# Performance work log

Measured on AMD Instinct MI355X. Metric: run time of the kernel, lower is better.

The kernel has to match this reference:

```python
import jax, jax.numpy as jnp
import numpy as np

LN_EPS = 1e-5


def setup_inputs() -> dict:
    key = jax.random.key(0)
    ks = jax.random.split(key, 4)
    B, L, Dm, N = 16, 2048, 512, 64
    return {
        "x": jax.random.normal(ks[0], (B, L, Dm), dtype=jnp.float32),
        "A": jax.random.normal(ks[1], (Dm, N), dtype=jnp.float32),
        "C": jax.random.normal(ks[2], (Dm, N), dtype=jnp.float32),
        "D": jax.random.normal(ks[3], (Dm,), dtype=jnp.float32),
        "gamma": jnp.ones((Dm,), dtype=jnp.float32),
        "beta": jnp.zeros((Dm,), dtype=jnp.float32),
    }


def reference(x, A, C, D, gamma, beta):
    # LayerNorm over last dim (matches nn.LayerNorm(d_model))
    mean = jnp.mean(x, axis=-1, keepdims=True)
    var = jnp.mean(jnp.square(x - mean), axis=-1, keepdims=True)
    x_norm = (x - mean) * jax.lax.rsqrt(var + LN_EPS) * gamma + beta

    B, L, Dm = x.shape
    N = A.shape[1]
    h0 = jnp.zeros((B, N), dtype=x.dtype)

    def step(h, u):
        # u: [B, Dm]; h: [B, N]
        h = jnp.tanh(u @ A + h)
        y = h @ C.T + u * D  # [B, Dm]
        return h, y

    # scan over time: xs [L, B, Dm]
    _, ys = jax.lax.scan(step, h0, jnp.swapaxes(x_norm, 0, 1))
    out = jnp.swapaxes(ys, 0, 1)  # [B, L, Dm]
    return out + x
```

## Files before the change

kernel.cpp:

```cpp
#include <hip/hip_runtime.h>
#include <hip/hip_bf16.h>

typedef short bf16x8 __attribute__((ext_vector_type(8)));
typedef float f32x4 __attribute__((ext_vector_type(4)));

constexpr int B_ = 16;
constexpr int L_ = 2048;
constexpr int DM = 512;
constexpr int NS = 64;
constexpr int BL = B_ * L_;
constexpr float LN_EPS = 1e-5f;
constexpr float KLN = 2.8853900817779268f;

constexpr int SEGS = 32;
constexpr int LSEG = L_ / SEGS;
constexpr int WARM = 64;

__device__ __forceinline__ unsigned f32bits(float f) {
    union { float f; unsigned u; } v{f}; return v.u;
}
__device__ __forceinline__ float bitsf32(unsigned u) {
    union { unsigned u; float f; } v{u}; return v.f;
}
__device__ __forceinline__ unsigned short f2bf(float f) {
    unsigned u = f32bits(f);
    unsigned r = u + 0x7FFF + ((u >> 16) & 1);
    return (unsigned short)(r >> 16);
}

__device__ __forceinline__ void norm_split8(float4 u0, float4 u1,
                                            float rstd, float m2,
                                            bf16x8& ah, bf16x8& al) {
    float t[8] = { fmaf(u0.x, rstd, m2), fmaf(u0.y, rstd, m2),
                   fmaf(u0.z, rstd, m2), fmaf(u0.w, rstd, m2),
                   fmaf(u1.x, rstd, m2), fmaf(u1.y, rstd, m2),
                   fmaf(u1.z, rstd, m2), fmaf(u1.w, rstd, m2) };
    unsigned hb[8], lb[8];
    #pragma unroll
    for (int j = 0; j < 8; ++j) {
        unsigned tb = f32bits(t[j]);
        hb[j] = tb & 0xFFFF0000u;
        lb[j] = f32bits(t[j] - bitsf32(hb[j]));
    }
    union { unsigned u[4]; bf16x8 v; } H, L;
    #pragma unroll
    for (int p = 0; p < 4; ++p) {
        H.u[p] = (hb[2*p] >> 16) | hb[2*p+1];
        L.u[p] = (lb[2*p] >> 16) | (lb[2*p+1] & 0xFFFF0000u);
    }
    ah = H.v; al = L.v;
}

__global__ __launch_bounds__(256) void k_pack(const float* __restrict__ A,
                                              const float* __restrict__ C,
                                              const float* __restrict__ gamma,
                                              const float* __restrict__ beta,
                                              const float* __restrict__ Dv,
                                              unsigned short* __restrict__ PAh,
                                              unsigned short* __restrict__ PAl,
                                              unsigned short* __restrict__ PC2,
                                              float* __restrict__ c0,
                                              float* __restrict__ gd,
                                              float* __restrict__ bd) {
    const int blk = blockIdx.x;
    const int tid = threadIdx.x;
    if (blk < 32) {
        const int g = blk * 256 + tid;
        if (g < 4096) {
            const int lane = g & 63, ct = (g >> 6) & 3, k32 = (g >> 8) & 3, kc = g >> 10;
            const int kbase = kc * 128 + k32 * 32 + (lane >> 4) * 8;
            const int col   = ct * 16 + (lane & 15);
            unsigned hb[8], lb[8];
            #pragma unroll
            for (int j = 0; j < 8; ++j) {
                float v = gamma[kbase + j] * A[(size_t)(kbase + j) * NS + col];
                unsigned tb = f32bits(v);
                hb[j] = tb & 0xFFFF0000u;
                lb[j] = f32bits(v - bitsf32(hb[j]));
            }
            uint4 ph, pl;
            ph.x = (hb[0] >> 16) | hb[1]; ph.y = (hb[2] >> 16) | hb[3];
            ph.z = (hb[4] >> 16) | hb[5]; ph.w = (hb[6] >> 16) | hb[7];
            pl.x = (lb[0] >> 16) | (lb[1] & 0xFFFF0000u);
            pl.y = (lb[2] >> 16) | (lb[3] & 0xFFFF0000u);
            pl.z = (lb[4] >> 16) | (lb[5] & 0xFFFF0000u);
            pl.w = (lb[6] >> 16) | (lb[7] & 0xFFFF0000u);
            *reinterpret_cast<uint4*>(PAh + (size_t)g * 8) = ph;
            *reinterpret_cast<uint4*>(PAl + (size_t)g * 8) = pl;
        } else {
            const int g2   = g - 4096;
            const int lane = g2 & 63;
            const int kt   = (g2 >> 6) & 1;
            const int offs = (g2 >> 7) & 1;
            const int dblk = g2 >> 8;
            const int i    = lane & 15;
            const int d    = dblk * 32 + ((i >> 2) * 8) + offs * 4 + (i & 3);
            const int nb   = kt * 32 + (lane >> 4) * 8;
            unsigned short v[8];
            #pragma unroll
            for (int j = 0; j < 8; ++j) v[j] = f2bf(C[(size_t)d * NS + nb + j]);
            uint4 p;
            p.x = v[0] | ((unsigned)v[1] << 16); p.y = v[2] | ((unsigned)v[3] << 16);
            p.z = v[4] | ((unsigned)v[5] << 16); p.w = v[6] | ((unsigned)v[7] << 16);
            *reinterpret_cast<uint4*>(PC2 + (size_t)g2 * 8) = p;
        }
    } else {
        __shared__ float red[256];
        #pragma unroll
        for (int i = 0; i < 2; ++i) {
            int d = tid + 256 * i;
            gd[d] = gamma[d] * Dv[d];
            bd[d] = beta[d] * Dv[d];
        }
        const int n = tid & 63, part = tid >> 6;
        float s = 0.f;
        #pragma unroll 8
        for (int k = part * 128; k < part * 128 + 128; ++k)
            s += beta[k] * A[(size_t)k * NS + n];
        red[tid] = s;
        __syncthreads();
        if (tid < 64)
            c0[tid] = red[tid] + red[tid + 64] + red[tid + 128] + red[tid + 192];
    }
}

__global__ __launch_bounds__(256) void k_gemmA(const float* __restrict__ x,
                                               const unsigned short* __restrict__ PAh,
                                               const unsigned short* __restrict__ PAl,
                                               const float* __restrict__ c0,
                                               float* __restrict__ stats,
                                               float* __restrict__ Bu) {
    const int tid  = threadIdx.x;
    const int r0   = blockIdx.x * 64;
    const int w    = tid >> 6;
    const int lane = tid & 63;
    const int myrow = 16 * w + (lane & 15);
    const int kb    = (lane >> 4) * 8;
    const float* xrow = x + (size_t)(r0 + myrow) * DM;

    float s = 0.f, s2 = 0.f;
    #pragma unroll
    for (int kc = 0; kc < 4; ++kc) {
        #pragma unroll
        for (int k32 = 0; k32 < 4; ++k32) {
            float4 a = *reinterpret_cast<const float4*>(xrow + kc * 128 + k32 * 32 + kb);
            float4 b = *reinterpret_cast<const float4*>(xrow + kc * 128 + k32 * 32 + kb + 4);
            s  += (a.x + a.y) + (a.z + a.w) + (b.x + b.y) + (b.z + b.w);
            s2 += a.x*a.x + a.y*a.y + a.z*a.z + a.w*a.w
                + b.x*b.x + b.y*b.y + b.z*b.z + b.w*b.w;
        }
    }
    s += __shfl_xor(s, 16); s2 += __shfl_xor(s2, 16);
    s += __shfl_xor(s, 32); s2 += __shfl_xor(s2, 32);
    const float mean = s * (1.0f / DM);
    const float var  = s2 * (1.0f / DM) - mean * mean;
    const float rstd = rsqrtf(var + LN_EPS);
    const float m2   = -mean * rstd;
    if (lane < 16) {
        stats[2 * (r0 + myrow)]     = mean;
        stats[2 * (r0 + myrow) + 1] = rstd;
    }

    f32x4 acc[4] = {};
    const bf16x8* ABh = reinterpret_cast<const bf16x8*>(PAh);
    const bf16x8* ABl = reinterpret_cast<const bf16x8*>(PAl);
    #pragma unroll
    for (int kc = 0; kc < 4; ++kc) {
        #pragma unroll
        for (int k32 = 0; k32 < 4; ++k32) {
            float4 u0 = *reinterpret_cast<const float4*>(xrow + kc * 128 + k32 * 32 + kb);
            float4 u1 = *reinterpret_cast<const float4*>(xrow + kc * 128 + k32 * 32 + kb + 4);
            bf16x8 ah, al;
            norm_split8(u0, u1, rstd, m2, ah, al);
            #pragma unroll
            for (int ct = 0; ct < 4; ++ct) {
                const int fi = ((kc * 4 + k32) * 4 + ct) * 64 + lane;
                bf16x8 bh = ABh[fi];
                bf16x8 bl = ABl[fi];
                acc[ct] = __builtin_amdgcn_mfma_f32_16x16x32_bf16(ah, bh, acc[ct], 0, 0, 0);
                acc[ct] = __builtin_amdgcn_mfma_f32_16x16x32_bf16(ah, bl, acc[ct], 0, 0, 0);
                acc[ct] = __builtin_amdgcn_mfma_f32_16x16x32_bf16(al, bh, acc[ct], 0, 0, 0);
            }
        }
    }

    const int orow = r0 + 16 * w + (lane >> 4) * 4;
    #pragma unroll
    for (int ct = 0; ct < 4; ++ct) {
        const int n = ct * 16 + (lane & 15);
        const float c0n = c0[n];
        #pragma unroll
        for (int j = 0; j < 4; ++j)
            Bu[(size_t)(orow + j) * NS + n] = acc[ct][j] + c0n;
    }
}

__global__ __launch_bounds__(512, 4) void k_scanC(const float* __restrict__ x,
                                                  const unsigned short* __restrict__ PC2,
                                                  const float* __restrict__ gd,
                                                  const float* __restrict__ bd,
                                                  const float* __restrict__ stats,
                                                  const float* __restrict__ Bu,
                                                  float* __restrict__ out) {
    __shared__ __align__(16) char smem[8192 + 4096];
    const int tid = threadIdx.x;
    const int seg = blockIdx.x & (SEGS - 1);
    const int b   = blockIdx.x >> 5;
    const int l0  = seg * LSEG;
    const int rowbase = b * L_ + l0;

    if (tid < 64) {
        constexpr int G = 16;
        const int n     = tid;
        const int start = (seg == 0) ? 0 : (l0 - WARM);
        const int skip  = l0 - start;
        const int nGrp  = (l0 + LSEG - start) / G;
        const float* bp = Bu + ((size_t)b * L_ + start) * NS + n;
        char* hbase = smem;

        float bufA[G], bufB[G];
        #pragma unroll
        for (int j = 0; j < G; ++j) bufA[j] = KLN * bp[(size_t)j * NS];
        float hv = 0.0f;
        int g = 0;
        for (;;) {
            {
                if (g + 1 < nGrp) {
                    const int base = (g + 1) * G;
                    #pragma unroll
                    for (int j = 0; j < G; ++j)
                        bufB[j] = KLN * bp[(size_t)(base + j) * NS];
                }
                const int lbase = g * G - skip;
                const bool doStore = lbase >= 0;
                #pragma unroll
                for (int j = 0; j < G; ++j) {
                    float t = fmaf(hv, KLN, bufA[j]);
                    float e = __builtin_amdgcn_exp2f(t);
                    float rr = __builtin_amdgcn_rcpf(e + 1.0f);
                    hv = fmaf(-2.0f, rr, 1.0f);
                    if (doStore) {
                        const int lr = lbase + j;
                        *reinterpret_cast<unsigned short*>(
                            hbase + lr * 128 + ((2 * n) ^ ((lr & 7) << 4))) = f2bf(hv);
                    }
                }
            }
            if (++g == nGrp) break;
            {
                if (g + 1 < nGrp) {
                    const int base = (g + 1) * G;
                    #pragma unroll
                    for (int j = 0; j < G; ++j)
                        bufA[j] = KLN * bp[(size_t)(base + j) * NS];
                }
                const int lbase = g * G - skip;
                const bool doStore = lbase >= 0;
                #pragma unroll
                for (int j = 0; j < G; ++j) {
                    float t = fmaf(hv, KLN, bufB[j]);
                    float e = __builtin_amdgcn_exp2f(t);
                    float rr = __builtin_amdgcn_rcpf(e + 1.0f);
                    hv = fmaf(-2.0f, rr, 1.0f);
                    if (doStore) {
                        const int lr = lbase + j;
                        *reinterpret_cast<unsigned short*>(
                            hbase + lr * 128 + ((2 * n) ^ ((lr & 7) << 4))) = f2bf(hv);
                    }
                }
            }
            if (++g == nGrp) break;
        }
    } else {
        float* GdS = (float*)(smem + 8192);
        const int t2 = tid - 64;
        if (t2 < 256)
            reinterpret_cast<float4*>(GdS)[t2] =
                (t2 < 128) ? reinterpret_cast<const float4*>(gd)[t2]
                           : reinterpret_cast<const float4*>(bd)[t2 - 128];
    }
    __syncthreads();

    const int w    = tid >> 6;
    const int lane = tid & 63;
    const int rg   = w & 3;
    const int half = w >> 2;
    const int hr   = rg * 16 + (lane & 15);
    const int kb   = (lane >> 4) * 8;
    const int grow = rowbase + hr;
    const float mean = stats[2 * grow];
    const float rstd = stats[2 * grow + 1];

    bf16x8 hfr0 = *reinterpret_cast<const bf16x8*>(
        smem + hr * 128 + (((lane >> 4) * 16) ^ ((hr & 7) << 4)));
    bf16x8 hfr1 = *reinterpret_cast<const bf16x8*>(
        smem + hr * 128 + ((64 + (lane >> 4) * 16) ^ ((hr & 7) << 4)));

    const float* GdS = (const float*)(smem + 8192);
    const float* BdS = GdS + DM;
    const float* xrp = x + (size_t)grow * DM;
    float* orp = out + (size_t)grow * DM;

    #pragma unroll
    for (int i = 0; i < 8; ++i) {
        const int dblk = half * 8 + i;
        bf16x8 c00 = *reinterpret_cast<const bf16x8*>(PC2 + ((size_t)dblk * 256 + lane) * 8);
        bf16x8 c01 = *reinterpret_cast<const bf16x8*>(PC2 + ((size_t)dblk * 256 + 64 + lane) * 8);
        bf16x8 c10 = *reinterpret_cast<const bf16x8*>(PC2 + ((size_t)dblk * 256 + 128 + lane) * 8);
        bf16x8 c11 = *reinterpret_cast<const bf16x8*>(PC2 + ((size_t)dblk * 256 + 192 + lane) * 8);
        f32x4 a0 = {}, a1 = {};
        a0 = __builtin_amdgcn_mfma_f32_16x16x32_bf16(c00, hfr0, a0, 0, 0, 0);
        a0 = __builtin_amdgcn_mfma_f32_16x16x32_bf16(c01, hfr1, a0, 0, 0, 0);
        a1 = __builtin_amdgcn_mfma_f32_16x16x32_bf16(c10, hfr0, a1, 0, 0, 0);
        a1 = __builtin_amdgcn_mfma_f32_16x16x32_bf16(c11, hfr1, a1, 0, 0, 0);

        const int db = dblk * 32 + kb;
        const float4 x0 = *reinterpret_cast<const float4*>(xrp + db);
        const float4 x1 = *reinterpret_cast<const float4*>(xrp + db + 4);
        const float4 g0 = *reinterpret_cast<const float4*>(GdS + db);
        const float4 g1 = *reinterpret_cast<const float4*>(GdS + db + 4);
        const float4 d0 = *reinterpret_cast<const float4*>(BdS + db);
        const float4 d1 = *reinterpret_cast<const float4*>(BdS + db + 4);
        float4 o0, o1;
        o0.x = fmaf((x0.x - mean) * rstd, g0.x, a0[0] + d0.x + x0.x);
        o0.y = fmaf((x0.y - mean) * rstd, g0.y, a0[1] + d0.y + x0.y);
        o0.z = fmaf((x0.z - mean) * rstd, g0.z, a0[2] + d0.z + x0.z);
        o0.w = fmaf((x0.w - mean) * rstd, g0.w, a0[3] + d0.w + x0.w);
        o1.x = fmaf((x1.x - mean) * rstd, g1.x, a1[0] + d1.x + x1.x);
        o1.y = fmaf((x1.y - mean) * rstd, g1.y, a1[1] + d1.y + x1.y);
        o1.z = fmaf((x1.z - mean) * rstd, g1.z, a1[2] + d1.z + x1.z);
        o1.w = fmaf((x1.w - mean) * rstd, g1.w, a1[3] + d1.w + x1.w);
        *reinterpret_cast<float4*>(orp + db)     = o0;
        *reinterpret_cast<float4*>(orp + db + 4) = o1;
    }
}

extern "C" void kernel_launch(void* const* d_in, const int* in_sizes, int n_in,
                              void* d_out, int out_size, void* d_ws, size_t ws_size,
                              hipStream_t stream) {
    const float* x     = (const float*)d_in[0];
    const float* A     = (const float*)d_in[1];
    const float* C     = (const float*)d_in[2];
    const float* Dv    = (const float*)d_in[3];
    const float* gamma = (const float*)d_in[4];
    const float* beta  = (const float*)d_in[5];
    float* out = (float*)d_out;

    char* ws = (char*)d_ws;
    float* Bu           = (float*)(ws);
    float* stats        = (float*)(ws + (size_t)BL * NS * 4);
    char* p = ws + (size_t)BL * NS * 4 + (size_t)BL * 2 * 4;
    unsigned short* PAh = (unsigned short*)p;        p += (size_t)DM * NS * 2;
    unsigned short* PAl = (unsigned short*)p;        p += (size_t)DM * NS * 2;
    unsigned short* PC2 = (unsigned short*)p;        p += (size_t)DM * NS * 2;
    float* c0           = (float*)p;                 p += 256;
    float* gd           = (float*)p;                 p += (size_t)DM * 4;
    float* bd           = (float*)p;

    k_pack<<<33, 256, 0, stream>>>(A, C, gamma, beta, Dv, PAh, PAl, PC2, c0, gd, bd);
    k_gemmA<<<BL / 64, 256, 0, stream>>>(x, PAh, PAl, c0, stats, Bu);
    k_scanC<<<B_ * SEGS, 512, 0, stream>>>(x, PC2, gd, bd, stats, Bu, out);
}
```

Before: 68.93 us.

## Fuse LayerNorm/A-projection GEMM into scan kernel, keeping Bu and stats in LDS

Merges the A-projection GEMM kernel into the segmented scan kernel. Each block computes LayerNorm statistics and the projection for its segment plus warm-up rows directly into shared memory, then runs the recurrence and the C-projection epilogue. This removes the global round trip of Bu and stats and one kernel launch. In exchange the warm-up rows' GEMM is recomputed per segment (128 rows instead of 64), LDS use grows to about 47KB per block which may lower occupancy, and the GEMM phase now serialises with the scan inside each block.

```diff
diff --git a/kernel.cpp b/kernel.cpp
--- a/kernel.cpp
+++ b/kernel.cpp
@@ -124,114 +124,111 @@
     }
 }
 
-__global__ __launch_bounds__(256) void k_gemmA(const float* __restrict__ x,
-                                               const unsigned short* __restrict__ PAh,
-                                               const unsigned short* __restrict__ PAl,
-                                               const float* __restrict__ c0,
-                                               float* __restrict__ stats,
-                                               float* __restrict__ Bu) {
+__global__ __launch_bounds__(512, 4) void k_all(const float* __restrict__ x,
+                                                const unsigned short* __restrict__ PAh,
+                                                const unsigned short* __restrict__ PAl,
+                                                const unsigned short* __restrict__ PC2,
+                                                const float* __restrict__ c0,
+                                                const float* __restrict__ gd,
+                                                const float* __restrict__ bd,
+                                                float* __restrict__ out) {
+    __shared__ __align__(16) char smem[33792 + 8192 + 4096 + 1024];
+    float* BuS          = (float*)smem;
+    char*  hbase        = smem + 33792;
+    float* GdS          = (float*)(smem + 33792 + 8192);
+    float* BdS          = GdS + DM;
+    float* statsS       = (float*)(smem + 33792 + 8192 + 4096);
+
     const int tid  = threadIdx.x;
-    const int r0   = blockIdx.x * 64;
+    const int blk  = blockIdx.x;
+    const int seg  = blk & (SEGS - 1);
+    const int b    = blk >> 5;
+    const int l0   = seg * LSEG;
+    const int lstart   = (seg == 0) ? 0 : (l0 - WARM);
+    const int nrows    = l0 + LSEG - lstart;
+    const int liveBase = nrows - 64;
+
     const int w    = tid >> 6;
     const int lane = tid & 63;
     const int myrow = 16 * w + (lane & 15);
     const int kb    = (lane >> 4) * 8;
-    const float* xrow = x + (size_t)(r0 + myrow) * DM;
-
-    float s = 0.f, s2 = 0.f;
-    #pragma unroll
-    for (int kc = 0; kc < 4; ++kc) {
-        #pragma unroll
-        for (int k32 = 0; k32 < 4; ++k32) {
-            float4 a = *reinterpret_cast<const float4*>(xrow + kc * 128 + k32 * 32 + kb);
-            float4 b = *reinterpret_cast<const float4*>(xrow + kc * 128 + k32 * 32 + kb + 4);
-            s  += (a.x + a.y) + (a.z + a.w) + (b.x + b.y) + (b.z + b.w);
-            s2 += a.x*a.x + a.y*a.y + a.z*a.z + a.w*a.w
-                + b.x*b.x + b.y*b.y + b.z*b.z + b.w*b.w;
-        }
-    }
-    s += __shfl_xor(s, 16); s2 += __shfl_xor(s2, 16);
-    s += __shfl_xor(s, 32); s2 += __shfl_xor(s2, 32);
-    const float mean = s * (1.0f / DM);
-    const float var  = s2 * (1.0f / DM) - mean * mean;
-    const float rstd = rsqrtf(var + LN_EPS);
-    const float m2   = -mean * rstd;
-    if (lane < 16) {
-        stats[2 * (r0 + myrow)]     = mean;
-        stats[2 * (r0 + myrow) + 1] = rstd;
-    }
-
-    f32x4 acc[4] = {};
-    const bf16x8* ABh = reinterpret_cast<const bf16x8*>(PAh);
-    const bf16x8* ABl = reinterpret_cast<const bf16x8*>(PAl);
-    #pragma unroll
-    for (int kc = 0; kc < 4; ++kc) {
-        #pragma unroll
-        for (int k32 = 0; k32 < 4; ++k32) {
-            float4 u0 = *reinterpret_cast<const float4*>(xrow + kc * 128 + k32 * 32 + kb);
-            float4 u1 = *reinterpret_cast<const float4*>(xrow + kc * 128 + k32 * 32 + kb + 4);
-            bf16x8 ah, al;
-            norm_split8(u0, u1, rstd, m2, ah, al);
-            #pragma unroll
-            for (int ct = 0; ct < 4; ++ct) {
-                const int fi = ((kc * 4 + k32) * 4 + ct) * 64 + lane;
-                bf16x8 bh = ABh[fi];
-                bf16x8 bl = ABl[fi];
-                acc[ct] = __builtin_amdgcn_mfma_f32_16x16x32_bf16(ah, bh, acc[ct], 0, 0, 0);
-                acc[ct] = __builtin_amdgcn_mfma_f32_16x16x32_bf16(ah, bl, acc[ct], 0, 0, 0);
-                acc[ct] = __builtin_amdgcn_mfma_f32_16x16x32_bf16(al, bh, acc[ct], 0, 0, 0);
-            }
-        }
-    }
-
-    const int orow = r0 + 16 * w + (lane >> 4) * 4;
-    #pragma unroll
-    for (int ct = 0; ct < 4; ++ct) {
-        const int n = ct * 16 + (lane & 15);
-        const float c0n = c0[n];
-        #pragma unroll
-        for (int j = 0; j < 4; ++j)
-            Bu[(size_t)(orow + j) * NS + n] = acc[ct][j] + c0n;
-    }
-}
-
-__global__ __launch_bounds__(512, 4) void k_scanC(const float* __restrict__ x,
-                                                  const unsigned short* __restrict__ PC2,
-                                                  const float* __restrict__ gd,
-                                                  const float* __restrict__ bd,
-                                                  const float* __restrict__ stats,
-                                                  const float* __restrict__ Bu,
-                                                  float* __restrict__ out) {
-    __shared__ __align__(16) char smem[8192 + 4096];
-    const int tid = threadIdx.x;
-    const int seg = blockIdx.x & (SEGS - 1);
-    const int b   = blockIdx.x >> 5;
-    const int l0  = seg * LSEG;
-    const int rowbase = b * L_ + l0;
-
-    if (tid < 64) {
+
+    if (w * 16 < nrows) {
+        const float* xrow = x + ((size_t)b * L_ + lstart + myrow) * DM;
+
+        float s = 0.f, s2 = 0.f;
+        #pragma unroll
+        for (int kc = 0; kc < 4; ++kc) {
+            #pragma unroll
+            for (int k32 = 0; k32 < 4; ++k32) {
+                float4 a = *reinterpret_cast<const float4*>(xrow + kc * 128 + k32 * 32 + kb);
+                float4 bq = *reinterpret_cast<const float4*>(xrow + kc * 128 + k32 * 32 + kb + 4);
+                s  += (a.x + a.y) + (a.z + a.w) + (bq.x + bq.y) + (bq.z + bq.w);
+                s2 += a.x*a.x + a.y*a.y + a.z*a.z + a.w*a.w
+                    + bq.x*bq.x + bq.y*bq.y + bq.z*bq.z + bq.w*bq.w;
+            }
+        }
+        s += __shfl_xor(s, 16); s2 += __shfl_xor(s2, 16);
+        s += __shfl_xor(s, 32); s2 += __shfl_xor(s2, 32);
+        const float mean = s * (1.0f / DM);
+        const float var  = s2 * (1.0f / DM) - mean * mean;
+        const float rstd = rsqrtf(var + LN_EPS);
+        const float m2   = -mean * rstd;
+        if (lane < 16) {
+            statsS[2 * myrow]     = mean;
+            statsS[2 * myrow + 1] = rstd;
+        }
+
+        f32x4 acc[4] = {};
+        const bf16x8* ABh = reinterpret_cast<const bf16x8*>(PAh);
+        const bf16x8* ABl = reinterpret_cast<const bf16x8*>(PAl);
+        #pragma unroll
+        for (int kc = 0; kc < 4; ++kc) {
+            #pragma unroll
+            for (int k32 = 0; k32 < 4; ++k32) {
+                float4 u0 = *reinterpret_cast<const float4*>(xrow + kc * 128 + k32 * 32 + kb);
+                float4 u1 = *reinterpret_cast<const float4*>(xrow + kc * 128 + k32 * 32 + kb + 4);
+                bf16x8 ah, al;
+                norm_split8(u0, u1, rstd, m2, ah, al);
+                #pragma unroll
+                for (int ct = 0; ct < 4; ++ct) {
+                    const int fi = ((kc * 4 + k32) * 4 + ct) * 64 + lane;
+                    bf16x8 bh = ABh[fi];
+                    bf16x8 bl = ABl[fi];
+                    acc[ct] = __builtin_amdgcn_mfma_f32_16x16x32_bf16(ah, bh, acc[ct], 0, 0, 0);
+                    acc[ct] = __builtin_amdgcn_mfma_f32_16x16x32_bf16(ah, bl, acc[ct], 0, 0, 0);
+                    acc[ct] = __builtin_amdgcn_mfma_f32_16x16x32_bf16(al, bh, acc[ct], 0, 0, 0);
+                }
+            }
+        }
+        const int orow = 16 * w + (lane >> 4) * 4;
+        #pragma unroll
+        for (int ct = 0; ct < 4; ++ct) {
+            const int n = ct * 16 + (lane & 15);
+            const float c0n = c0[n];
+            #pragma unroll
+            for (int j = 0; j < 4; ++j)
+                BuS[(orow + j) * 66 + n] = acc[ct][j] + c0n;
+        }
+    }
+    __syncthreads();
+
+    if (w == 0) {
         constexpr int G = 16;
-        const int n     = tid;
-        const int start = (seg == 0) ? 0 : (l0 - WARM);
-        const int skip  = l0 - start;
-        const int nGrp  = (l0 + LSEG - start) / G;
-        const float* bp = Bu + ((size_t)b * L_ + start) * NS + n;
-        char* hbase = smem;
-
+        const int nGrp = nrows / G;
         float bufA[G], bufB[G];
         #pragma unroll
-        for (int j = 0; j < G; ++j) bufA[j] = KLN * bp[(size_t)j * NS];
+        for (int j = 0; j < G; ++j) bufA[j] = KLN * BuS[j * 66 + lane];
         float hv = 0.0f;
         int g = 0;
         for (;;) {
             {
                 if (g + 1 < nGrp) {
-                    const int base = (g + 1) * G;
                     #pragma unroll
                     for (int j = 0; j < G; ++j)
-                        bufB[j] = KLN * bp[(size_t)(base + j) * NS];
-                }
-                const int lbase = g * G - skip;
+                        bufB[j] = KLN * BuS[((g + 1) * G + j) * 66 + lane];
+                }
+                const int lbase = g * G - liveBase;
                 const bool doStore = lbase >= 0;
                 #pragma unroll
                 for (int j = 0; j < G; ++j) {
@@ -242,19 +239,18 @@
                     if (doStore) {
                         const int lr = lbase + j;
                         *reinterpret_cast<unsigned short*>(
-                            hbase + lr * 128 + ((2 * n) ^ ((lr & 7) << 4))) = f2bf(hv);
+                            hbase + lr * 128 + ((2 * lane) ^ ((lr & 7) << 4))) = f2bf(hv);
                     }
                 }
             }
             if (++g == nGrp) break;
             {
                 if (g + 1 < nGrp) {
-                    const int base = (g + 1) * G;
                     #pragma unroll
                     for (int j = 0; j < G; ++j)
-                        bufA[j] = KLN * bp[(size_t)(base + j) * NS];
-                }
-                const int lbase = g * G - skip;
+                        bufA[j] = KLN * BuS[((g + 1) * G + j) * 66 + lane];
+                }
+                const int lbase = g * G - liveBase;
                 const bool doStore = lbase >= 0;
                 #pragma unroll
                 for (int j = 0; j < G; ++j) {
@@ -265,14 +261,13 @@
                     if (doStore) {
                         const int lr = lbase + j;
                         *reinterpret_cast<unsigned short*>(
-                            hbase + lr * 128 + ((2 * n) ^ ((lr & 7) << 4))) = f2bf(hv);
+                            hbase + lr * 128 + ((2 * lane) ^ ((lr & 7) << 4))) = f2bf(hv);
                     }
                 }
             }
             if (++g == nGrp) break;
         }
     } else {
-        float* GdS = (float*)(smem + 8192);
         const int t2 = tid - 64;
         if (t2 < 256)
             reinterpret_cast<float4*>(GdS)[t2] =
@@ -281,25 +276,20 @@
     }
     __syncthreads();
 
-    const int w    = tid >> 6;
-    const int lane = tid & 63;
     const int rg   = w & 3;
     const int half = w >> 2;
     const int hr   = rg * 16 + (lane & 15);
-    const int kb   = (lane >> 4) * 8;
-    const int grow = rowbase + hr;
-    const float mean = stats[2 * grow];
-    const float rstd = stats[2 * grow + 1];
+    const size_t grow = (size_t)b * L_ + l0 + hr;
+    const float mean = statsS[2 * (liveBase + hr)];
+    const float rstd = statsS[2 * (liveBase + hr) + 1];
 
     bf16x8 hfr0 = *reinterpret_cast<const bf16x8*>(
-        smem + hr * 128 + (((lane >> 4) * 16) ^ ((hr & 7) << 4)));
+        hbase + hr * 128 + (((lane >> 4) * 16) ^ ((hr & 7) << 4)));
     bf16x8 hfr1 = *reinterpret_cast<const bf16x8*>(
-        smem + hr * 128 + ((64 + (lane >> 4) * 16) ^ ((hr & 7) << 4)));
-
-    const float* GdS = (const float*)(smem + 8192);
-    const float* BdS = GdS + DM;
-    const float* xrp = x + (size_t)grow * DM;
-    float* orp = out + (size_t)grow * DM;
+        hbase + hr * 128 + ((64 + (lane >> 4) * 16) ^ ((hr & 7) << 4)));
+
+    const float* xrp = x + grow * DM;
+    float* orp = out + grow * DM;
 
     #pragma unroll
     for (int i = 0; i < 8; ++i) {
@@ -346,10 +336,7 @@
     const float* beta  = (const float*)d_in[5];
     float* out = (float*)d_out;
 
-    char* ws = (char*)d_ws;
-    float* Bu           = (float*)(ws);
-    float* stats        = (float*)(ws + (size_t)BL * NS * 4);
-    char* p = ws + (size_t)BL * NS * 4 + (size_t)BL * 2 * 4;
+    char* p = (char*)d_ws;
     unsigned short* PAh = (unsigned short*)p;        p += (size_t)DM * NS * 2;
     unsigned short* PAl = (unsigned short*)p;        p += (size_t)DM * NS * 2;
     unsigned short* PC2 = (unsigned short*)p;        p += (size_t)DM * NS * 2;
@@ -358,6 +345,5 @@
     float* bd           = (float*)p;
 
     k_pack<<<33, 256, 0, stream>>>(A, C, gamma, beta, Dv, PAh, PAl, PC2, c0, gd, bd);
-    k_gemmA<<<BL / 64, 256, 0, stream>>>(x, PAh, PAl, c0, stats, Bu);
-    k_scanC<<<B_ * SEGS, 512, 0, stream>>>(x, PC2, gd, bd, stats, Bu, out);
-}
+    k_all<<<B_ * SEGS, 512, 0, stream>>>(x, PAh, PAl, PC2, c0, gd, bd, out);
+}
```

After: 87.18 us, median of 2. +26.5%, slower.

## Split fused scan+C-projection into separate scan and GEMM kernels, cache x in registers

Applied to the files above, without the earlier changes.

Splits the fused scan/C-projection kernel into a 64-thread scan kernel that writes bf16 hidden states to global memory and a separate wide GEMM kernel for the output projection. The fused version left most threads idle during the serial scan, and the split is meant to let the output GEMM run at full occupancy. In exchange it adds a global round trip for h and an extra launch. Separately, k_gemmA now loads each x row once into registers and reuses it for both the LayerNorm stats and the MFMA pass, with a launch-bounds hint, and output stores become nontemporal.

```diff
diff --git a/kernel.cpp b/kernel.cpp
--- a/kernel.cpp
+++ b/kernel.cpp
@@ -124,7 +124,7 @@
     }
 }
 
-__global__ __launch_bounds__(256) void k_gemmA(const float* __restrict__ x,
+__global__ __launch_bounds__(256, 2) void k_gemmA(const float* __restrict__ x,
                                                const unsigned short* __restrict__ PAh,
                                                const unsigned short* __restrict__ PAl,
                                                const float* __restrict__ c0,
@@ -138,17 +138,24 @@
     const int kb    = (lane >> 4) * 8;
     const float* xrow = x + (size_t)(r0 + myrow) * DM;
 
-    float s = 0.f, s2 = 0.f;
+    float4 xv[32];
     #pragma unroll
     for (int kc = 0; kc < 4; ++kc) {
         #pragma unroll
         for (int k32 = 0; k32 < 4; ++k32) {
-            float4 a = *reinterpret_cast<const float4*>(xrow + kc * 128 + k32 * 32 + kb);
-            float4 b = *reinterpret_cast<const float4*>(xrow + kc * 128 + k32 * 32 + kb + 4);
-            s  += (a.x + a.y) + (a.z + a.w) + (b.x + b.y) + (b.z + b.w);
-            s2 += a.x*a.x + a.y*a.y + a.z*a.z + a.w*a.w
-                + b.x*b.x + b.y*b.y + b.z*b.z + b.w*b.w;
-        }
+            xv[kc * 8 + 2 * k32]     = *reinterpret_cast<const float4*>(
+                xrow + kc * 128 + k32 * 32 + kb);
+            xv[kc * 8 + 2 * k32 + 1] = *reinterpret_cast<const float4*>(
+                xrow + kc * 128 + k32 * 32 + kb + 4);
+        }
+    }
+
+    float s = 0.f, s2 = 0.f;
+    #pragma unroll
+    for (int i = 0; i < 32; ++i) {
+        float4 a = xv[i];
+        s  += (a.x + a.y) + (a.z + a.w);
+        s2 += a.x*a.x + a.y*a.y + a.z*a.z + a.w*a.w;
     }
     s += __shfl_xor(s, 16); s2 += __shfl_xor(s2, 16);
     s += __shfl_xor(s, 32); s2 += __shfl_xor(s2, 32);
@@ -168,10 +175,8 @@
     for (int kc = 0; kc < 4; ++kc) {
         #pragma unroll
         for (int k32 = 0; k32 < 4; ++k32) {
-            float4 u0 = *reinterpret_cast<const float4*>(xrow + kc * 128 + k32 * 32 + kb);
-            float4 u1 = *reinterpret_cast<const float4*>(xrow + kc * 128 + k32 * 32 + kb + 4);
             bf16x8 ah, al;
-            norm_split8(u0, u1, rstd, m2, ah, al);
+            norm_split8(xv[kc * 8 + 2 * k32], xv[kc * 8 + 2 * k32 + 1], rstd, m2, ah, al);
             #pragma unroll
             for (int ct = 0; ct < 4; ++ct) {
                 const int fi = ((kc * 4 + k32) * 4 + ct) * 64 + lane;
@@ -195,111 +200,91 @@
     }
 }
 
-__global__ __launch_bounds__(512, 4) void k_scanC(const float* __restrict__ x,
+__global__ __launch_bounds__(64) void k_scan(const float* __restrict__ Bu,
+                                             unsigned short* __restrict__ h) {
+    constexpr int G = 16;
+    const int seg = blockIdx.x & (SEGS - 1);
+    const int b   = blockIdx.x / SEGS;
+    const int n   = threadIdx.x;
+    const int l0     = seg * LSEG;
+    const int start  = (seg == 0) ? 0 : (l0 - WARM);
+    const int skip   = l0 - start;
+    const int nGrp   = (l0 + LSEG - start) / G;
+
+    const float* bp = Bu + ((size_t)b * L_ + start) * NS + n;
+    unsigned short* hp = h + ((size_t)b * L_ + start) * NS + n;
+
+    float bufA[G], bufB[G];
+    #pragma unroll
+    for (int j = 0; j < G; ++j) bufA[j] = KLN * bp[(size_t)j * NS];
+
+    float hv = 0.0f;
+    int g = 0;
+    for (;;) {
+        {
+            if (g + 1 < nGrp) {
+                const int base = (g + 1) * G;
+                #pragma unroll
+                for (int j = 0; j < G; ++j)
+                    bufB[j] = KLN * bp[(size_t)(base + j) * NS];
+            }
+            const bool doStore = g * G >= skip;
+            unsigned short* hq = hp + (size_t)(g * G) * NS;
+            #pragma unroll
+            for (int j = 0; j < G; ++j) {
+                float t = fmaf(hv, KLN, bufA[j]);
+                float e = __builtin_amdgcn_exp2f(t);
+                float rr = __builtin_amdgcn_rcpf(e + 1.0f);
+                hv = fmaf(-2.0f, rr, 1.0f);
+                if (doStore) hq[(size_t)j * NS] = f2bf(hv);
+            }
+        }
+        if (++g == nGrp) break;
+        {
+            if (g + 1 < nGrp) {
+                const int base = (g + 1) * G;
+                #pragma unroll
+                for (int j = 0; j < G; ++j)
+                    bufA[j] = KLN * bp[(size_t)(base + j) * NS];
+            }
+            const bool doStore = g * G >= skip;
+            unsigned short* hq = hp + (size_t)(g * G) * NS;
+            #pragma unroll
+            for (int j = 0; j < G; ++j) {
+                float t = fmaf(hv, KLN, bufB[j]);
+                float e = __builtin_amdgcn_exp2f(t);
+                float rr = __builtin_amdgcn_rcpf(e + 1.0f);
+                hv = fmaf(-2.0f, rr, 1.0f);
+                if (doStore) hq[(size_t)j * NS] = f2bf(hv);
+            }
+        }
+        if (++g == nGrp) break;
+    }
+}
+
+__global__ __launch_bounds__(256, 4) void k_gemmC(const float* __restrict__ x,
                                                   const unsigned short* __restrict__ PC2,
                                                   const float* __restrict__ gd,
                                                   const float* __restrict__ bd,
                                                   const float* __restrict__ stats,
-                                                  const float* __restrict__ Bu,
+                                                  const unsigned short* __restrict__ h,
                                                   float* __restrict__ out) {
-    __shared__ __align__(16) char smem[8192 + 4096];
-    const int tid = threadIdx.x;
-    const int seg = blockIdx.x & (SEGS - 1);
-    const int b   = blockIdx.x >> 5;
-    const int l0  = seg * LSEG;
-    const int rowbase = b * L_ + l0;
-
-    if (tid < 64) {
-        constexpr int G = 16;
-        const int n     = tid;
-        const int start = (seg == 0) ? 0 : (l0 - WARM);
-        const int skip  = l0 - start;
-        const int nGrp  = (l0 + LSEG - start) / G;
-        const float* bp = Bu + ((size_t)b * L_ + start) * NS + n;
-        char* hbase = smem;
-
-        float bufA[G], bufB[G];
-        #pragma unroll
-        for (int j = 0; j < G; ++j) bufA[j] = KLN * bp[(size_t)j * NS];
-        float hv = 0.0f;
-        int g = 0;
-        for (;;) {
-            {
-                if (g + 1 < nGrp) {
-                    const int base = (g + 1) * G;
-                    #pragma unroll
-                    for (int j = 0; j < G; ++j)
-                        bufB[j] = KLN * bp[(size_t)(base + j) * NS];
-                }
-                const int lbase = g * G - skip;
-                const bool doStore = lbase >= 0;
-                #pragma unroll
-                for (int j = 0; j < G; ++j) {
-                    float t = fmaf(hv, KLN, bufA[j]);
-                    float e = __builtin_amdgcn_exp2f(t);
-                    float rr = __builtin_amdgcn_rcpf(e + 1.0f);
-                    hv = fmaf(-2.0f, rr, 1.0f);
-                    if (doStore) {
-                        const int lr = lbase + j;
-                        *reinterpret_cast<unsigned short*>(
-                            hbase + lr * 128 + ((2 * n) ^ ((lr & 7) << 4))) = f2bf(hv);
-                    }
-                }
-            }
-            if (++g == nGrp) break;
-            {
-                if (g + 1 < nGrp) {
-                    const int base = (g + 1) * G;
-                    #pragma unroll
-                    for (int j = 0; j < G; ++j)
-                        bufA[j] = KLN * bp[(size_t)(base + j) * NS];
-                }
-                const int lbase = g * G - skip;
-                const bool doStore = lbase >= 0;
-                #pragma unroll
-                for (int j = 0; j < G; ++j) {
-                    float t = fmaf(hv, KLN, bufB[j]);
-                    float e = __builtin_amdgcn_exp2f(t);
-                    float rr = __builtin_amdgcn_rcpf(e + 1.0f);
-                    hv = fmaf(-2.0f, rr, 1.0f);
-                    if (doStore) {
-                        const int lr = lbase + j;
-                        *reinterpret_cast<unsigned short*>(
-                            hbase + lr * 128 + ((2 * n) ^ ((lr & 7) << 4))) = f2bf(hv);
-                    }
-                }
-            }
-            if (++g == nGrp) break;
-        }
-    } else {
-        float* GdS = (float*)(smem + 8192);
-        const int t2 = tid - 64;
-        if (t2 < 256)
-            reinterpret_cast<float4*>(GdS)[t2] =
-                (t2 < 128) ? reinterpret_cast<const float4*>(gd)[t2]
-                           : reinterpret_cast<const float4*>(bd)[t2 - 128];
-    }
-    __syncthreads();
-
+    const int tid  = threadIdx.x;
+    const int rt   = blockIdx.x >> 1;
+    const int half = blockIdx.x & 1;
     const int w    = tid >> 6;
     const int lane = tid & 63;
-    const int rg   = w & 3;
-    const int half = w >> 2;
-    const int hr   = rg * 16 + (lane & 15);
     const int kb   = (lane >> 4) * 8;
-    const int grow = rowbase + hr;
+
+    const size_t grow = (size_t)rt * 64 + w * 16 + (lane & 15);
     const float mean = stats[2 * grow];
     const float rstd = stats[2 * grow + 1];
 
-    bf16x8 hfr0 = *reinterpret_cast<const bf16x8*>(
-        smem + hr * 128 + (((lane >> 4) * 16) ^ ((hr & 7) << 4)));
-    bf16x8 hfr1 = *reinterpret_cast<const bf16x8*>(
-        smem + hr * 128 + ((64 + (lane >> 4) * 16) ^ ((hr & 7) << 4)));
-
-    const float* GdS = (const float*)(smem + 8192);
-    const float* BdS = GdS + DM;
-    const float* xrp = x + (size_t)grow * DM;
-    float* orp = out + (size_t)grow * DM;
+    bf16x8 hfr0 = *reinterpret_cast<const bf16x8*>(h + grow * NS + kb);
+    bf16x8 hfr1 = *reinterpret_cast<const bf16x8*>(h + grow * NS + 32 + kb);
+
+    const float* xrp = x + grow * DM;
+    float* orp = out + grow * DM;
 
     #pragma unroll
     for (int i = 0; i < 8; ++i) {
@@ -317,21 +302,21 @@
         const int db = dblk * 32 + kb;
         const float4 x0 = *reinterpret_cast<const float4*>(xrp + db);
         const float4 x1 = *reinterpret_cast<const float4*>(xrp + db + 4);
-        const float4 g0 = *reinterpret_cast<const float4*>(GdS + db);
-        const float4 g1 = *reinterpret_cast<const float4*>(GdS + db + 4);
-        const float4 d0 = *reinterpret_cast<const float4*>(BdS + db);
-        const float4 d1 = *reinterpret_cast<const float4*>(BdS + db + 4);
-        float4 o0, o1;
-        o0.x = fmaf((x0.x - mean) * rstd, g0.x, a0[0] + d0.x + x0.x);
-        o0.y = fmaf((x0.y - mean) * rstd, g0.y, a0[1] + d0.y + x0.y);
-        o0.z = fmaf((x0.z - mean) * rstd, g0.z, a0[2] + d0.z + x0.z);
-        o0.w = fmaf((x0.w - mean) * rstd, g0.w, a0[3] + d0.w + x0.w);
-        o1.x = fmaf((x1.x - mean) * rstd, g1.x, a1[0] + d1.x + x1.x);
-        o1.y = fmaf((x1.y - mean) * rstd, g1.y, a1[1] + d1.y + x1.y);
-        o1.z = fmaf((x1.z - mean) * rstd, g1.z, a1[2] + d1.z + x1.z);
-        o1.w = fmaf((x1.w - mean) * rstd, g1.w, a1[3] + d1.w + x1.w);
-        *reinterpret_cast<float4*>(orp + db)     = o0;
-        *reinterpret_cast<float4*>(orp + db + 4) = o1;
+        const float4 g0 = *reinterpret_cast<const float4*>(gd + db);
+        const float4 g1 = *reinterpret_cast<const float4*>(gd + db + 4);
+        const float4 d0 = *reinterpret_cast<const float4*>(bd + db);
+        const float4 d1 = *reinterpret_cast<const float4*>(bd + db + 4);
+        f32x4 o0, o1;
+        o0[0] = fmaf((x0.x - mean) * rstd, g0.x, a0[0] + d0.x + x0.x);
+        o0[1] = fmaf((x0.y - mean) * rstd, g0.y, a0[1] + d0.y + x0.y);
+        o0[2] = fmaf((x0.z - mean) * rstd, g0.z, a0[2] + d0.z + x0.z);
+        o0[3] = fmaf((x0.w - mean) * rstd, g0.w, a0[3] + d0.w + x0.w);
+        o1[0] = fmaf((x1.x - mean) * rstd, g1.x, a1[0] + d1.x + x1.x);
+        o1[1] = fmaf((x1.y - mean) * rstd, g1.y, a1[1] + d1.y + x1.y);
+        o1[2] = fmaf((x1.z - mean) * rstd, g1.z, a1[2] + d1.z + x1.z);
+        o1[3] = fmaf((x1.w - mean) * rstd, g1.w, a1[3] + d1.w + x1.w);
+        __builtin_nontemporal_store(o0, reinterpret_cast<f32x4*>(orp + db));
+        __builtin_nontemporal_store(o1, reinterpret_cast<f32x4*>(orp + db + 4));
     }
 }
 
@@ -346,10 +331,10 @@
     const float* beta  = (const float*)d_in[5];
     float* out = (float*)d_out;
 
-    char* ws = (char*)d_ws;
-    float* Bu           = (float*)(ws);
-    float* stats        = (float*)(ws + (size_t)BL * NS * 4);
-    char* p = ws + (size_t)BL * NS * 4 + (size_t)BL * 2 * 4;
+    char* p = (char*)d_ws;
+    float* Bu           = (float*)p;                 p += (size_t)BL * NS * 4;
+    unsigned short* h   = (unsigned short*)p;        p += (size_t)BL * NS * 2;
+    float* stats        = (float*)p;                 p += (size_t)BL * 2 * 4;
     unsigned short* PAh = (unsigned short*)p;        p += (size_t)DM * NS * 2;
     unsigned short* PAl = (unsigned short*)p;        p += (size_t)DM * NS * 2;
     unsigned short* PC2 = (unsigned short*)p;        p += (size_t)DM * NS * 2;
@@ -359,5 +344,6 @@
 
     k_pack<<<33, 256, 0, stream>>>(A, C, gamma, beta, Dv, PAh, PAl, PC2, c0, gd, bd);
     k_gemmA<<<BL / 64, 256, 0, stream>>>(x, PAh, PAl, c0, stats, Bu);
-    k_scanC<<<B_ * SEGS, 512, 0, stream>>>(x, PC2, gd, bd, stats, Bu, out);
-}
+    k_scan<<<B_ * SEGS, 64, 0, stream>>>(Bu, h);
+    k_gemmC<<<(BL / 64) * 2, 256, 0, stream>>>(x, PC2, gd, bd, stats, h, out);
+}
```

Measured after the change: 78.13 us. 1.13x slower.

## Double scan segments to 64 and cache x rows in registers in gemmA

Applied to the files above, without the earlier changes.

The scan kernel now splits each sequence into 64 segments of 32 steps instead of 32 of 64. This doubles the block count and halves the serial recurrence each block runs, at the cost of relatively more warm-up recomputation. The output phase is rebalanced to 32 rows per block, with each warp covering a quarter of the model dimension. Separately, k_gemmA loads each x row slice once into 32 float4 registers and reuses them for both the statistics and the normalise/MFMA pass, avoiding a second global read. It adds a launch-bounds occupancy hint to offset the higher register pressure.

```diff
diff --git a/kernel.cpp b/kernel.cpp
--- a/kernel.cpp
+++ b/kernel.cpp
@@ -12,7 +12,7 @@
 constexpr float LN_EPS = 1e-5f;
 constexpr float KLN = 2.8853900817779268f;
 
-constexpr int SEGS = 32;
+constexpr int SEGS = 64;
 constexpr int LSEG = L_ / SEGS;
 constexpr int WARM = 64;
 
@@ -124,7 +124,7 @@
     }
 }
 
-__global__ __launch_bounds__(256) void k_gemmA(const float* __restrict__ x,
+__global__ __launch_bounds__(256, 2) void k_gemmA(const float* __restrict__ x,
                                                const unsigned short* __restrict__ PAh,
                                                const unsigned short* __restrict__ PAl,
                                                const float* __restrict__ c0,
@@ -138,17 +138,24 @@
     const int kb    = (lane >> 4) * 8;
     const float* xrow = x + (size_t)(r0 + myrow) * DM;
 
+    float4 xv[32];
+    #pragma unroll
+    for (int kc = 0; kc < 4; ++kc) {
+        #pragma unroll
+        for (int k32 = 0; k32 < 4; ++k32) {
+            xv[kc * 8 + 2 * k32]     = *reinterpret_cast<const float4*>(
+                xrow + kc * 128 + k32 * 32 + kb);
+            xv[kc * 8 + 2 * k32 + 1] = *reinterpret_cast<const float4*>(
+                xrow + kc * 128 + k32 * 32 + kb + 4);
+        }
+    }
+
     float s = 0.f, s2 = 0.f;
     #pragma unroll
-    for (int kc = 0; kc < 4; ++kc) {
-        #pragma unroll
-        for (int k32 = 0; k32 < 4; ++k32) {
-            float4 a = *reinterpret_cast<const float4*>(xrow + kc * 128 + k32 * 32 + kb);
-            float4 b = *reinterpret_cast<const float4*>(xrow + kc * 128 + k32 * 32 + kb + 4);
-            s  += (a.x + a.y) + (a.z + a.w) + (b.x + b.y) + (b.z + b.w);
-            s2 += a.x*a.x + a.y*a.y + a.z*a.z + a.w*a.w
-                + b.x*b.x + b.y*b.y + b.z*b.z + b.w*b.w;
-        }
+    for (int i = 0; i < 32; ++i) {
+        float4 a = xv[i];
+        s  += (a.x + a.y) + (a.z + a.w);
+        s2 += a.x*a.x + a.y*a.y + a.z*a.z + a.w*a.w;
     }
     s += __shfl_xor(s, 16); s2 += __shfl_xor(s2, 16);
     s += __shfl_xor(s, 32); s2 += __shfl_xor(s2, 32);
@@ -168,10 +175,8 @@
     for (int kc = 0; kc < 4; ++kc) {
         #pragma unroll
         for (int k32 = 0; k32 < 4; ++k32) {
-            float4 u0 = *reinterpret_cast<const float4*>(xrow + kc * 128 + k32 * 32 + kb);
-            float4 u1 = *reinterpret_cast<const float4*>(xrow + kc * 128 + k32 * 32 + kb + 4);
             bf16x8 ah, al;
-            norm_split8(u0, u1, rstd, m2, ah, al);
+            norm_split8(xv[kc * 8 + 2 * k32], xv[kc * 8 + 2 * k32 + 1], rstd, m2, ah, al);
             #pragma unroll
             for (int ct = 0; ct < 4; ++ct) {
                 const int fi = ((kc * 4 + k32) * 4 + ct) * 64 + lane;
@@ -202,17 +207,17 @@
                                                   const float* __restrict__ stats,
                                                   const float* __restrict__ Bu,
                                                   float* __restrict__ out) {
-    __shared__ __align__(16) char smem[8192 + 4096];
+    __shared__ __align__(16) char smem[4096 + 4096];
     const int tid = threadIdx.x;
     const int seg = blockIdx.x & (SEGS - 1);
-    const int b   = blockIdx.x >> 5;
+    const int b   = blockIdx.x >> 6;
     const int l0  = seg * LSEG;
     const int rowbase = b * L_ + l0;
 
     if (tid < 64) {
         constexpr int G = 16;
         const int n     = tid;
-        const int start = (seg == 0) ? 0 : (l0 - WARM);
+        const int start = (l0 > WARM) ? (l0 - WARM) : 0;
         const int skip  = l0 - start;
         const int nGrp  = (l0 + LSEG - start) / G;
         const float* bp = Bu + ((size_t)b * L_ + start) * NS + n;
@@ -272,7 +277,7 @@
             if (++g == nGrp) break;
         }
     } else {
-        float* GdS = (float*)(smem + 8192);
+        float* GdS = (float*)(smem + 4096);
         const int t2 = tid - 64;
         if (t2 < 256)
             reinterpret_cast<float4*>(GdS)[t2] =
@@ -283,11 +288,11 @@
 
     const int w    = tid >> 6;
     const int lane = tid & 63;
-    const int rg   = w & 3;
-    const int half = w >> 2;
+    const int rg   = w & 1;
+    const int q    = w >> 1;
     const int hr   = rg * 16 + (lane & 15);
     const int kb   = (lane >> 4) * 8;
-    const int grow = rowbase + hr;
+    const size_t grow = (size_t)rowbase + hr;
     const float mean = stats[2 * grow];
     const float rstd = stats[2 * grow + 1];
 
@@ -296,14 +301,14 @@
     bf16x8 hfr1 = *reinterpret_cast<const bf16x8*>(
         smem + hr * 128 + ((64 + (lane >> 4) * 16) ^ ((hr & 7) << 4)));
 
-    const float* GdS = (const float*)(smem + 8192);
+    const float* GdS = (const float*)(smem + 4096);
     const float* BdS = GdS + DM;
-    const float* xrp = x + (size_t)grow * DM;
-    float* orp = out + (size_t)grow * DM;
-
-    #pragma unroll
-    for (int i = 0; i < 8; ++i) {
-        const int dblk = half * 8 + i;
+    const float* xrp = x + grow * DM;
+    float* orp = out + grow * DM;
+
+    #pragma unroll
+    for (int i = 0; i < 4; ++i) {
+        const int dblk = q * 4 + i;
         bf16x8 c00 = *reinterpret_cast<const bf16x8*>(PC2 + ((size_t)dblk * 256 + lane) * 8);
         bf16x8 c01 = *reinterpret_cast<const bf16x8*>(PC2 + ((size_t)dblk * 256 + 64 + lane) * 8);
         bf16x8 c10 = *reinterpret_cast<const bf16x8*>(PC2 + ((size_t)dblk * 256 + 128 + lane) * 8);
@@ -346,10 +351,9 @@
     const float* beta  = (const float*)d_in[5];
     float* out = (float*)d_out;
 
-    char* ws = (char*)d_ws;
-    float* Bu           = (float*)(ws);
-    float* stats        = (float*)(ws + (size_t)BL * NS * 4);
-    char* p = ws + (size_t)BL * NS * 4 + (size_t)BL * 2 * 4;
+    char* p = (char*)d_ws;
+    float* Bu           = (float*)p;                 p += (size_t)BL * NS * 4;
+    float* stats        = (float*)p;                 p += (size_t)BL * 2 * 4;
     unsigned short* PAh = (unsigned short*)p;        p += (size_t)DM * NS * 2;
     unsigned short* PAl = (unsigned short*)p;        p += (size_t)DM * NS * 2;
     unsigned short* PC2 = (unsigned short*)p;        p += (size_t)DM * NS * 2;
```

New measurement: 72.71 us. 5.5% more time.
